# Kernel optimization log

Measured on AMD Instinct MI355X. Metric: run time of the kernel, lower is better.

## Reference

```python
import jax, jax.numpy as jnp
import numpy as np

SEQ, BATCH, HID, OUT = 2048, 128, 256, 2

def setup_inputs() -> dict:
    key = jax.random.key(0)
    ks = jax.random.split(key, 6)
    return {
        "x": jax.random.normal(ks[0], (SEQ, BATCH), dtype=jnp.float32),
        # torch code draws h inside forward: randn*0.01 + 0.5 -> pass as input for determinism
        "h0": jax.random.normal(ks[1], (BATCH, HID), dtype=jnp.float32) * 0.01 + 0.5,
        "W_ih": jax.random.normal(ks[2], (HID, 1), dtype=jnp.float32) * 0.05 + 0.4,
        "W_hh": jax.random.normal(ks[3], (HID, HID), dtype=jnp.float32) * 0.2,
        "W_hh_bias": jax.random.normal(ks[4], (HID, HID), dtype=jnp.float32) * 0.01 + 0.5,
        "b_h": jnp.zeros((HID,), dtype=jnp.float32),
        "W": jax.random.normal(ks[5], (OUT, HID), dtype=jnp.float32) * 0.1 + 0.5,
        "b": jnp.zeros((OUT,), dtype=jnp.float32),
        "context": 1,
    }

def reference(x, h0, W_ih, W_hh, W_hh_bias, b_h, W, b, context):
    # context is a scalar, so c1 + c2 = (2h-1) @ (W_hh + context*W_hh_bias).T (same math, one GEMM)
    W_eff = W_hh + context * W_hh_bias            # (hid, hid)
    w_in = W_ih[:, 0]                             # input_size == 1 -> (hid,)

    def step(h, x_t):
        # c0: (batch,1)@(1,hid) == outer product of x_t with W_ih column
        pre = x_t[:, None] * w_in[None, :] + (2.0 * h - 1.0) @ W_eff.T + b_h
        h_new = jax.nn.sigmoid(pre)
        return h_new, h_new

    _, hs = jax.lax.scan(step, h0, x)             # hs: (seq, batch, hid)
    out = jnp.transpose(hs, (1, 0, 2))            # (batch, seq, hid)
    y = out @ W.T + b                             # (batch, seq, out)
    return y[:, :, 0], out
```

## Files before the change

### kernel.cpp

```cpp
#include <hip/hip_runtime.h>
#include <math.h>

#define SEQ   2048
#define BATCH 128
#define HID   256
#define NCH   16
#define KCH   16
#define VST   20

template <int CTRL>
__device__ __forceinline__ float dpp_mov(float x) {
    return __int_as_float(__builtin_amdgcn_update_dpp(
        __float_as_int(x), __float_as_int(x), CTRL, 0xF, 0xF, false));
}
__device__ __forceinline__ float swz_xor4(float x) {
    return __int_as_float(__builtin_amdgcn_ds_swizzle(__float_as_int(x), 0x101F));
}

__global__ __launch_bounds__(512) __attribute__((amdgpu_waves_per_eu(2, 2)))
void rnn_scan_kernel(const float* __restrict__ x,
                     const float* __restrict__ h0,
                     const float* __restrict__ W_ih,
                     const float* __restrict__ W_hh,
                     const float* __restrict__ W_hh_b,
                     const float* __restrict__ b_h,
                     const int*   __restrict__ context,
                     float*       __restrict__ out_hs)
{
    const int b   = blockIdx.x;
    const int tid = threadIdx.x;
    const int R   = tid >> 4;
    const int l   = tid & 15;
    const int l7  = tid & 7;
    const int row = 8 * R + l7;

    __shared__ __align__(16) float v_lds[2][NCH * VST];
    __shared__ float x_lds[SEQ];

    for (int t = tid; t < SEQ; t += 512)
        x_lds[t] = x[t * BATCH + b];

    const float ctx = (float)context[0];

    float4 wreg[8][4];
    #pragma unroll
    for (int j = 0; j < 8; ++j) {
        const int rj = 8 * R + (l7 ^ j);
        const float* wp = W_hh   + (size_t)rj * HID + KCH * l;
        const float* bp = W_hh_b + (size_t)rj * HID + KCH * l;
        #pragma unroll
        for (int c = 0; c < 4; ++c) {
            const float4 a = *(const float4*)(wp + 4 * c);
            const float4 d = *(const float4*)(bp + 4 * c);
            wreg[j][c] = make_float4(a.x + ctx * d.x, a.y + ctx * d.y,
                                     a.z + ctx * d.z, a.w + ctx * d.w);
        }
    }

    const float winj = W_ih[row];
    const float bhj  = b_h[row];

    const int voff = VST * (row >> 4) + (row & 15);
    v_lds[0][voff] = 2.f * h0[(size_t)b * HID + row] - 1.f;

    float* outp = out_hs + (size_t)b * SEQ * HID + row;

    const float4* vr0 = (const float4*)(v_lds[0] + VST * l);
    const float4* vr1 = (const float4*)(v_lds[1] + VST * l);

    __syncthreads();

    auto step = [&](int t, const float4* __restrict__ vr, float* __restrict__ vw) {
        float q[8] = {0.f, 0.f, 0.f, 0.f, 0.f, 0.f, 0.f, 0.f};
        #pragma unroll
        for (int c = 0; c < 4; ++c) {
            const float4 v4 = vr[c];
            #pragma unroll
            for (int j = 0; j < 8; ++j) {
                const float4 w = wreg[j][c];
                q[j] += w.x * v4.x;
                q[j] += w.y * v4.y;
                q[j] += w.z * v4.z;
                q[j] += w.w * v4.w;
            }
        }
        #pragma unroll
        for (int j = 0; j < 8; ++j) q[j] += dpp_mov<0x128>(q[j]);
        q[0] += dpp_mov<0xB1>(q[1]);
        q[2] += dpp_mov<0xB1>(q[3]);
        q[4] += dpp_mov<0xB1>(q[5]);
        q[6] += dpp_mov<0xB1>(q[7]);
        q[0] += dpp_mov<0x4E>(q[2]);
        q[4] += dpp_mov<0x4E>(q[6]);
        q[0] += swz_xor4(q[4]);

        const float pre = q[0] + bhj + x_lds[t] * winj;
        const float h = 1.f / (1.f + __expf(-pre));
        vw[voff] = 2.f * h - 1.f;
        if ((tid & 8) == 0)
            outp[(size_t)t * HID] = h;
        __syncthreads();
    };

    for (int t = 0; t < SEQ; t += 2) {
        step(t,     vr0, v_lds[1]);
        step(t + 1, vr1, v_lds[0]);
    }
}

__global__ __launch_bounds__(256, 4)
void head_kernel(const float* __restrict__ hs,
                 const float* __restrict__ W,
                 const float* __restrict__ bias,
                 float*       __restrict__ y)
{
    const int tid  = threadIdx.x;
    const int lane = tid & 63;
    const int sub  = lane & 15;
    const int rsub = lane >> 4;

    float4 w0[4];
    #pragma unroll
    for (int u = 0; u < 4; ++u)
        w0[u] = *(const float4*)(W + 4 * (16 * u + sub));
    const float b0 = bias[0];

    const int gwave = (blockIdx.x * blockDim.x + tid) >> 6;
    const int nw    = (gridDim.x * blockDim.x) >> 6;
    const int nq    = (BATCH * SEQ) >> 2;

    for (int q = gwave; q < nq; q += nw) {
        const int rrow = q * 4 + rsub;
        const float* rp = hs + (size_t)rrow * HID;
        float s = 0.f;
        #pragma unroll
        for (int u = 0; u < 4; ++u) {
            const float4 hv = *(const float4*)(rp + 4 * (16 * u + sub));
            s += hv.x * w0[u].x + hv.y * w0[u].y +
                 hv.z * w0[u].z + hv.w * w0[u].w;
        }
        s += __shfl_xor(s, 1, 64);
        s += __shfl_xor(s, 2, 64);
        s += __shfl_xor(s, 4, 64);
        s += __shfl_xor(s, 8, 64);
        if (sub == 0) y[rrow] = s + b0;
    }
}

extern "C" void kernel_launch(void* const* d_in, const int* in_sizes, int n_in,
                              void* d_out, int out_size, void* d_ws, size_t ws_size,
                              hipStream_t stream) {
    const float* x      = (const float*)d_in[0];
    const float* h0     = (const float*)d_in[1];
    const float* W_ih   = (const float*)d_in[2];
    const float* W_hh   = (const float*)d_in[3];
    const float* W_hh_b = (const float*)d_in[4];
    const float* b_h    = (const float*)d_in[5];
    const float* W      = (const float*)d_in[6];
    const float* bias   = (const float*)d_in[7];
    const int*   ctx    = (const int*)d_in[8];

    float* y  = (float*)d_out;
    float* hs = y + (size_t)BATCH * SEQ;

    rnn_scan_kernel<<<BATCH, 512, 0, stream>>>(x, h0, W_ih, W_hh, W_hh_b,
                                               b_h, ctx, hs);
    head_kernel<<<2048, 256, 0, stream>>>(hs, W, bias, y);
}
```

Measured before the change: 1.443 ms.

## Fuse output head projection into recurrent scan kernel

Removes the separate head kernel, which re-read the full hidden-state tensor from memory. Each step of the scan now reduces h*W[0] across the block with DPP and swizzle operations, writes per-wave partials to double-buffered LDS, and has thread 0 sum them one step later. Asm pins on the weight registers are added to stop the compiler from rematerialising or spilling them. This adds serial work inside the latency-bound recurrence loop, in exchange for dropping one launch and a 256MB read.

Result: slower. 1.782 ms (+23.5%).

```diff
diff --git a/kernel.cpp b/kernel.cpp
--- a/kernel.cpp
+++ b/kernel.cpp
@@ -4,8 +4,6 @@
 #define SEQ   2048
 #define BATCH 128
 #define HID   256
-#define NCH   16
-#define KCH   16
 #define VST   20
 
 template <int CTRL>
@@ -13,9 +11,11 @@
     return __int_as_float(__builtin_amdgcn_update_dpp(
         __float_as_int(x), __float_as_int(x), CTRL, 0xF, 0xF, false));
 }
-__device__ __forceinline__ float swz_xor4(float x) {
-    return __int_as_float(__builtin_amdgcn_ds_swizzle(__float_as_int(x), 0x101F));
+template <int PAT>
+__device__ __forceinline__ float swz(float x) {
+    return __int_as_float(__builtin_amdgcn_ds_swizzle(__float_as_int(x), PAT));
 }
+#define PIN4(v) asm volatile("" : "+v"((v).x), "+v"((v).y), "+v"((v).z), "+v"((v).w))
 
 __global__ __launch_bounds__(512) __attribute__((amdgpu_waves_per_eu(2, 2)))
 void rnn_scan_kernel(const float* __restrict__ x,
@@ -24,7 +24,10 @@
                      const float* __restrict__ W_hh,
                      const float* __restrict__ W_hh_b,
                      const float* __restrict__ b_h,
+                     const float* __restrict__ W,
+                     const float* __restrict__ bias,
                      const int*   __restrict__ context,
+                     float*       __restrict__ y,
                      float*       __restrict__ out_hs)
 {
     const int b   = blockIdx.x;
@@ -34,7 +37,8 @@
     const int l7  = tid & 7;
     const int row = 8 * R + l7;
 
-    __shared__ __align__(16) float v_lds[2][NCH * VST];
+    __shared__ __align__(16) float v_lds[2][16 * VST];
+    __shared__ __align__(16) float ypart[2][16];
     __shared__ float x_lds[SEQ];
 
     for (int t = tid; t < SEQ; t += 512)
@@ -46,8 +50,8 @@
     #pragma unroll
     for (int j = 0; j < 8; ++j) {
         const int rj = 8 * R + (l7 ^ j);
-        const float* wp = W_hh   + (size_t)rj * HID + KCH * l;
-        const float* bp = W_hh_b + (size_t)rj * HID + KCH * l;
+        const float* wp = W_hh   + (size_t)rj * HID + 16 * l;
+        const float* bp = W_hh_b + (size_t)rj * HID + 16 * l;
         #pragma unroll
         for (int c = 0; c < 4; ++c) {
             const float4 a = *(const float4*)(wp + 4 * c);
@@ -59,18 +63,41 @@
 
     const float winj = W_ih[row];
     const float bhj  = b_h[row];
+    const float w0r  = W[row];
+    const float b0   = bias[0];
 
     const int voff = VST * (row >> 4) + (row & 15);
     v_lds[0][voff] = 2.f * h0[(size_t)b * HID + row] - 1.f;
 
     float* outp = out_hs + (size_t)b * SEQ * HID + row;
+    float* yp   = y + (size_t)b * SEQ;
 
     const float4* vr0 = (const float4*)(v_lds[0] + VST * l);
     const float4* vr1 = (const float4*)(v_lds[1] + VST * l);
 
     __syncthreads();
 
-    auto step = [&](int t, const float4* __restrict__ vr, float* __restrict__ vw) {
+    auto step = [&](int t, const float4* __restrict__ vr,
+                    float* __restrict__ vw,
+                    const float* __restrict__ ypr,
+                    float* __restrict__ ypw) {
+        #pragma unroll
+        for (int j = 0; j < 8; ++j) {
+            PIN4(wreg[j][0]); PIN4(wreg[j][1]);
+            PIN4(wreg[j][2]); PIN4(wreg[j][3]);
+        }
+
+        if (tid == 0 && t > 0) {
+            const float4 s0 = *(const float4*)(ypr + 0);
+            const float4 s1 = *(const float4*)(ypr + 4);
+            const float4 s2 = *(const float4*)(ypr + 8);
+            const float4 s3 = *(const float4*)(ypr + 12);
+            yp[t - 1] = b0 + (((s0.x + s0.y) + (s0.z + s0.w)) +
+                              ((s1.x + s1.y) + (s1.z + s1.w))) +
+                             (((s2.x + s2.y) + (s2.z + s2.w)) +
+                              ((s3.x + s3.y) + (s3.z + s3.w)));
+        }
+
         float q[8] = {0.f, 0.f, 0.f, 0.f, 0.f, 0.f, 0.f, 0.f};
         #pragma unroll
         for (int c = 0; c < 4; ++c) {
@@ -92,58 +119,41 @@
         q[6] += dpp_mov<0xB1>(q[7]);
         q[0] += dpp_mov<0x4E>(q[2]);
         q[4] += dpp_mov<0x4E>(q[6]);
-        q[0] += swz_xor4(q[4]);
+        q[0] += swz<0x101F>(q[4]);
 
         const float pre = q[0] + bhj + x_lds[t] * winj;
         const float h = 1.f / (1.f + __expf(-pre));
+
+        float yc = ((tid & 8) == 0) ? h * w0r : 0.f;
+        yc += dpp_mov<0xB1>(yc);
+        yc += dpp_mov<0x4E>(yc);
+        yc += swz<0x101F>(yc);
+        yc += dpp_mov<0x128>(yc);
+        yc += swz<0x401F>(yc);
+        if ((tid & 31) == 0) ypw[tid >> 5] = yc;
+
         vw[voff] = 2.f * h - 1.f;
         if ((tid & 8) == 0)
             outp[(size_t)t * HID] = h;
+
         __syncthreads();
     };
 
     for (int t = 0; t < SEQ; t += 2) {
-        step(t,     vr0, v_lds[1]);
-        step(t + 1, vr1, v_lds[0]);
+        step(t,     vr0, v_lds[1], ypart[1], ypart[0]);
+        step(t + 1, vr1, v_lds[0], ypart[0], ypart[1]);
     }
-}
 
-__global__ __launch_bounds__(256, 4)
-void head_kernel(const float* __restrict__ hs,
-                 const float* __restrict__ W,
-                 const float* __restrict__ bias,
-                 float*       __restrict__ y)
-{
-    const int tid  = threadIdx.x;
-    const int lane = tid & 63;
-    const int sub  = lane & 15;
-    const int rsub = lane >> 4;
-
-    float4 w0[4];
-    #pragma unroll
-    for (int u = 0; u < 4; ++u)
-        w0[u] = *(const float4*)(W + 4 * (16 * u + sub));
-    const float b0 = bias[0];
-
-    const int gwave = (blockIdx.x * blockDim.x + tid) >> 6;
-    const int nw    = (gridDim.x * blockDim.x) >> 6;
-    const int nq    = (BATCH * SEQ) >> 2;
-
-    for (int q = gwave; q < nq; q += nw) {
-        const int rrow = q * 4 + rsub;
-        const float* rp = hs + (size_t)rrow * HID;
-        float s = 0.f;
-        #pragma unroll
-        for (int u = 0; u < 4; ++u) {
-            const float4 hv = *(const float4*)(rp + 4 * (16 * u + sub));
-            s += hv.x * w0[u].x + hv.y * w0[u].y +
-                 hv.z * w0[u].z + hv.w * w0[u].w;
-        }
-        s += __shfl_xor(s, 1, 64);
-        s += __shfl_xor(s, 2, 64);
-        s += __shfl_xor(s, 4, 64);
-        s += __shfl_xor(s, 8, 64);
-        if (sub == 0) y[rrow] = s + b0;
+    if (tid == 0) {
+        const float* pp = ypart[(SEQ - 1) & 1];
+        const float4 s0 = *(const float4*)(pp + 0);
+        const float4 s1 = *(const float4*)(pp + 4);
+        const float4 s2 = *(const float4*)(pp + 8);
+        const float4 s3 = *(const float4*)(pp + 12);
+        yp[SEQ - 1] = b0 + (((s0.x + s0.y) + (s0.z + s0.w)) +
+                            ((s1.x + s1.y) + (s1.z + s1.w))) +
+                           (((s2.x + s2.y) + (s2.z + s2.w)) +
+                            ((s3.x + s3.y) + (s3.z + s3.w)));
     }
 }
 
@@ -164,6 +174,5 @@
     float* hs = y + (size_t)BATCH * SEQ;
 
     rnn_scan_kernel<<<BATCH, 512, 0, stream>>>(x, h0, W_ih, W_hh, W_hh_b,
-                                               b_h, ctx, hs);
-    head_kernel<<<2048, 256, 0, stream>>>(hs, W, bias, y);
+                                               b_h, W, bias, ctx, y, hs);
 }
```
